# Optimization experiments

Hardware: AMD Instinct MI355X
Metric: run time of the kernel (lower is better)

Reference implementation:

```python
import jax, jax.numpy as jnp
import numpy as np

B, N, D_IN, D_HID, D_OUT = 64, 512, 512, 512, 512


def setup_inputs() -> dict:
    key = jax.random.key(0)
    ks = jax.random.split(key, 8)
    gain = 0.02  # xavier_normal_ gain used in reset_parameters_xavier

    def xavier(k, fan_in, fan_out):
        std = gain * np.sqrt(2.0 / (fan_in + fan_out))
        return jax.random.normal(k, (fan_in, fan_out), dtype=jnp.float32) * std

    return {
        "batch_graph": jax.random.normal(ks[0], (B, N, D_IN), dtype=jnp.float32),
        "adj": jax.random.uniform(ks[1], (B, N, N), dtype=jnp.float32),
        "W1": xavier(ks[2], D_IN, D_HID),
        "b1": jnp.zeros((D_HID,), dtype=jnp.float32),
        "W2": xavier(ks[3], D_HID, D_HID),
        "b2": jnp.zeros((D_HID,), dtype=jnp.float32),
        "W3": xavier(ks[4], D_HID, D_OUT),
        "b3": jnp.zeros((D_OUT,), dtype=jnp.float32),
    }


def _normalize_adj(adj):
    # rowsum^-0.5 with inf -> 0 (original: torch.pow then isinf mask)
    rowsum = adj.sum(axis=1)                       # [B, N] (sum over dim 1, as in torch)
    safe = jnp.where(rowsum == 0, 1.0, rowsum)
    r = jnp.where(rowsum == 0, 0.0, safe ** -0.5)  # [B, N]
    # (adj @ D)^T @ D = D @ adj^T @ D with D = diag(r)
    return r[:, :, None] * jnp.swapaxes(adj, 1, 2) * r[:, None, :]


def reference(batch_graph, adj, W1, b1, W2, b2, W3, b3):
    # Block-diagonal big_adj @ big_graph == per-graph batched matmul.
    A = _normalize_adj(adj)  # [B, N, N]

    def gc(x, W, b):
        # support = x @ W ; output = A @ support + b
        return jnp.einsum('bij,bjd->bid', A, x @ W) + b

    # dropout is identity in eval mode (deterministic reference)
    x = jax.nn.relu(gc(batch_graph, W1, b1))
    x = jax.nn.relu(gc(x, W2, b2))
    return gc(x, W3, b3)  # [B, N, D_OUT]
```

## Files before the change

kernel.cpp:

```cpp
#include <hip/hip_runtime.h>
#include <cstdint>
#include <cstddef>

typedef _Float16 f16;
typedef _Float16 f16x4 __attribute__((ext_vector_type(4)));
typedef _Float16 f16x8 __attribute__((ext_vector_type(8)));
typedef float    f32x4 __attribute__((ext_vector_type(4)));

#define NB 64
#define NN 262144

__device__ __forceinline__ void gload_lds16(const void* g, void* l) {
    __builtin_amdgcn_global_load_lds(
        (const __attribute__((address_space(1))) void*)g,
        (__attribute__((address_space(3))) void*)l, 16, 0, 0);
}

__global__ void k_colsum_part(const float* __restrict__ adj, float* __restrict__ part) {
    int b = blockIdx.y, ch = blockIdx.x;
    const float* ab = adj + (size_t)b * NN + (size_t)ch * 32 * 512;
    int c = threadIdx.x;
    float s0 = 0.f, s1 = 0.f;
    #pragma unroll 8
    for (int i = 0; i < 32; ++i) {
        s0 += ab[i * 512 + c];
        s1 += ab[i * 512 + c + 256];
    }
    float* p = part + ((size_t)b * 16 + ch) * 512;
    p[c] = s0; p[c + 256] = s1;
}

__global__ void k_colsum_fin(const float* __restrict__ part, float* __restrict__ r) {
    int idx = blockIdx.x * 256 + threadIdx.x;
    int b = idx >> 9, n = idx & 511;
    const float* p = part + (size_t)b * 16 * 512 + n;
    float s = 0.f;
    #pragma unroll
    for (int ch = 0; ch < 16; ++ch) s += p[ch * 512];
    r[idx] = (s > 0.f) ? rsqrtf(s) : 0.f;
}

__global__ void k_makeA(const float* __restrict__ adj, const float* __restrict__ r,
                        f16* __restrict__ A_h) {
    __shared__ float t[64][65];
    int b = blockIdx.z;
    int i0 = blockIdx.y * 64, j0 = blockIdx.x * 64;
    const float* ab = adj + (size_t)b * NN;
    int c = threadIdx.x & 63, r4 = threadIdx.x >> 6;
    #pragma unroll
    for (int s = 0; s < 16; ++s) {
        int rr = r4 + s * 4;
        t[rr][c] = ab[(size_t)(j0 + rr) * 512 + i0 + c];
    }
    __syncthreads();
    const float* rb = r + (size_t)b * 512;
    f16* Ab = A_h + (size_t)b * NN;
    int jq = (threadIdx.x & 15) * 4;
    int ib = threadIdx.x >> 4;
    #pragma unroll
    for (int s = 0; s < 4; ++s) {
        int ii = ib + s * 16;
        float ri = 16.f * rb[i0 + ii];
        f16x4 o;
        #pragma unroll
        for (int q = 0; q < 4; ++q)
            o[q] = (f16)(ri * t[jq + q][ii] * rb[j0 + jq + q]);
        *(f16x4*)&Ab[(size_t)(i0 + ii) * 512 + j0 + jq] = o;
    }
}

__global__ void k_transW(const float* __restrict__ W1, const float* __restrict__ W2,
                         const float* __restrict__ W3, f16* __restrict__ Wt) {
    __shared__ float t[64][65];
    const float* W = blockIdx.z == 0 ? W1 : (blockIdx.z == 1 ? W2 : W3);
    f16* out = Wt + (size_t)blockIdx.z * NN;
    int k0 = blockIdx.y * 64, d0 = blockIdx.x * 64;
    int c = threadIdx.x & 63, r4 = threadIdx.x >> 6;
    #pragma unroll
    for (int s = 0; s < 16; ++s) {
        int rr = r4 + s * 4;
        t[rr][c] = W[(size_t)(k0 + rr) * 512 + d0 + c];
    }
    __syncthreads();
    int kq = (threadIdx.x & 15) * 4;
    int db = threadIdx.x >> 4;
    #pragma unroll
    for (int s = 0; s < 4; ++s) {
        int dd = db + s * 16;
        f16x4 o;
        #pragma unroll
        for (int q = 0; q < 4; ++q)
            o[q] = (f16)(64.f * t[kq + q][dd]);
        *(f16x4*)&out[(size_t)(d0 + dd) * 512 + k0 + kq] = o;
    }
}

__global__ void k_cvtX(const float* __restrict__ x, f16* __restrict__ xh) {
    size_t i = ((size_t)blockIdx.x * 256 + threadIdx.x) * 8;
    float4 v0 = *(const float4*)(x + i);
    float4 v1 = *(const float4*)(x + i + 4);
    f16x8 o;
    o[0] = (f16)v0.x; o[1] = (f16)v0.y; o[2] = (f16)v0.z; o[3] = (f16)v0.w;
    o[4] = (f16)v1.x; o[5] = (f16)v1.y; o[6] = (f16)v1.z; o[7] = (f16)v1.w;
    *(f16x8*)(xh + i) = o;
}

template<bool BIAS, bool RELU, bool OUTF32>
__global__ __launch_bounds__(512, 1)
void gemm_tn_ct(const f16* __restrict__ P, size_t pstr,
                const f16* __restrict__ Qt, size_t qstr,
                void* __restrict__ Cout, size_t cstr,
                const float* __restrict__ bias, float iscale, float oscale) {
    __shared__ __align__(16) f16 Plds[2][16384];
    __shared__ __align__(16) f16 Qlds[2][16384];

    const int tid  = threadIdx.x;
    const int lane = tid & 63;
    const int wid  = tid >> 6;
    const int wm   = wid >> 2;
    const int wn   = wid & 3;

    const int wg  = blockIdx.x;
    const int swz = (wg & 7) * 32 + (wg >> 3);
    const int b   = swz >> 2;
    const int tt  = swz & 3;
    const int m0  = (tt >> 1) * 256;
    const int n0  = (tt & 1) * 256;

    const f16* Pb = P + (size_t)b * pstr;
    const f16* Qb = Qt + (size_t)b * qstr;

    const int srow = tid >> 3;
    const int sswz = (tid & 7) ^ (srow & 7);

    const int fr  = lane & 15;
    const int fs  = lane >> 4;
    const int fx  = fr & 7;

    auto stage = [&](const f16* __restrict__ Gb, int row0, f16* lds, int k0) {
        #pragma unroll
        for (int r = 0; r < 4; ++r) {
            const f16* src = Gb + (size_t)(row0 + r * 64 + srow) * 512 + k0 + sswz * 8;
            gload_lds16(src, lds + r * 4096 + tid * 8);
        }
    };

    f32x4 acc[8][4] = {};

    stage(Pb, m0, &Plds[0][0], 0);
    stage(Qb, n0, &Qlds[0][0], 0);

    for (int t = 0; t < 8; ++t) {
        const int nb = t & 1;
        if (t < 7) {
            stage(Pb, m0, &Plds[nb ^ 1][0], (t + 1) * 64);
            stage(Qb, n0, &Qlds[nb ^ 1][0], (t + 1) * 64);
            asm volatile("s_waitcnt vmcnt(8)" ::: "memory");
        } else {
            asm volatile("s_waitcnt vmcnt(0)" ::: "memory");
        }
        __builtin_amdgcn_s_barrier();

        const f16* Pl = &Plds[nb][0];
        const f16* Ql = &Qlds[nb][0];
        #pragma unroll
        for (int krep = 0; krep < 2; ++krep) {
            const int s = fs + krep * 4;
            const int sp = (s ^ fx) * 8;
            f16x8 af[8], bf[4];
            #pragma unroll
            for (int mi = 0; mi < 8; ++mi)
                af[mi] = *(const f16x8*)&Pl[(wm * 128 + mi * 16 + fr) * 64 + sp];
            #pragma unroll
            for (int ni = 0; ni < 4; ++ni)
                bf[ni] = *(const f16x8*)&Ql[(wn * 64 + ni * 16 + fr) * 64 + sp];
            __builtin_amdgcn_s_setprio(1);
            #pragma unroll
            for (int mi = 0; mi < 8; ++mi)
                #pragma unroll
                for (int ni = 0; ni < 4; ++ni)
                    acc[mi][ni] = __builtin_amdgcn_mfma_f32_16x16x32_f16(
                        af[mi], bf[ni], acc[mi][ni], 0, 0, 0);
            __builtin_amdgcn_s_setprio(0);
        }
        asm volatile("s_waitcnt lgkmcnt(0)" ::: "memory");
        __builtin_amdgcn_sched_barrier(0);
        __builtin_amdgcn_s_barrier();
    }

    const int cmb = (lane >> 4) * 4;
    #pragma unroll
    for (int mi = 0; mi < 8; ++mi) {
        #pragma unroll
        for (int ni = 0; ni < 4; ++ni) {
            const int n = n0 + wn * 64 + ni * 16 + fr;
            const int m = m0 + wm * 128 + mi * 16 + cmb;
            float v[4];
            #pragma unroll
            for (int q = 0; q < 4; ++q) {
                float x = acc[mi][ni][q] * iscale;
                if (BIAS) x += bias[m + q];
                if (RELU) x = fmaxf(x, 0.f);
                v[q] = x * oscale;
            }
            if (OUTF32) {
                float* Cb = (float*)Cout + (size_t)b * cstr;
                f32x4 o; o[0] = v[0]; o[1] = v[1]; o[2] = v[2]; o[3] = v[3];
                *(f32x4*)&Cb[(size_t)n * 512 + m] = o;
            } else {
                f16* Cb = (f16*)Cout + (size_t)b * cstr;
                f16x4 o; o[0] = (f16)v[0]; o[1] = (f16)v[1]; o[2] = (f16)v[2]; o[3] = (f16)v[3];
                *(f16x4*)&Cb[(size_t)n * 512 + m] = o;
            }
        }
    }
}

extern "C" void kernel_launch(void* const* d_in, const int* in_sizes, int n_in,
                              void* d_out, int out_size, void* d_ws, size_t ws_size,
                              hipStream_t stream) {
    const float* X0  = (const float*)d_in[0];
    const float* adj = (const float*)d_in[1];
    const float* W1  = (const float*)d_in[2];
    const float* b1  = (const float*)d_in[3];
    const float* W2  = (const float*)d_in[4];
    const float* b2  = (const float*)d_in[5];
    const float* W3  = (const float*)d_in[6];
    const float* b3  = (const float*)d_in[7];

    uint8_t* ws = (uint8_t*)d_ws;
    float* rbuf = (float*)ws;
    f16* Wt1 = (f16*)(ws + 131072);
    f16* Wt2 = Wt1 + NN;
    f16* Wt3 = Wt2 + NN;
    f16* A_h = (f16*)(ws + 131072 + (size_t)3 * NN * 2);
    f16* X_h = A_h + (size_t)NB * NN;
    f16* S_t = X_h + (size_t)NB * NN;
    float* part = (float*)S_t;

    k_colsum_part<<<dim3(16, 64), dim3(256), 0, stream>>>(adj, part);
    k_colsum_fin <<<dim3(128),    dim3(256), 0, stream>>>(part, rbuf);
    k_makeA <<<dim3(8, 8, NB), dim3(256), 0, stream>>>(adj, rbuf, A_h);
    k_transW<<<dim3(8, 8, 3),  dim3(256), 0, stream>>>(W1, W2, W3, Wt1);
    k_cvtX  <<<dim3(8192),     dim3(256), 0, stream>>>(X0, X_h);

    dim3 gg(256), gb(512);
    gemm_tn_ct<false, false, false><<<gg, gb, 0, stream>>>(X_h, (size_t)NN, Wt1, (size_t)0,  S_t, (size_t)NN, nullptr, 1.f, 1.f / 64.f);
    gemm_tn_ct<true,  true,  false><<<gg, gb, 0, stream>>>(S_t, (size_t)NN, A_h, (size_t)NN, X_h, (size_t)NN, b1, 1.f / 16.f, 1.f);
    gemm_tn_ct<false, false, false><<<gg, gb, 0, stream>>>(X_h, (size_t)NN, Wt2, (size_t)0,  S_t, (size_t)NN, nullptr, 1.f, 4.f);
    gemm_tn_ct<true,  true,  false><<<gg, gb, 0, stream>>>(S_t, (size_t)NN, A_h, (size_t)NN, X_h, (size_t)NN, b2, 1.f / 4096.f, 256.f);
    gemm_tn_ct<false, false, false><<<gg, gb, 0, stream>>>(X_h, (size_t)NN, Wt3, (size_t)0,  S_t, (size_t)NN, nullptr, 1.f, 1.f / 64.f);
    gemm_tn_ct<true,  false, true ><<<gg, gb, 0, stream>>>(S_t, (size_t)NN, A_h, (size_t)NN, d_out, (size_t)NN, b3, 1.f / 4096.f, 1.f);
}
```

Before: 222.9 us.

## Shrink GEMM tiles to 128x128 with two blocks per CU and fuse prep kernels

Retiles the batched GEMM from 256x256 tiles with 512 threads and one block per CU to 128x128 tiles with 256 threads and two blocks per CU, launching 1024 blocks. The aim is better occupancy and latency hiding at the cost of lower operand reuse and more LDS/global traffic per flop. It also merges the X conversion, weight transpose and colsum finalize kernels into one launch that dispatches on block index, to cut launch overhead.

```diff
diff --git a/kernel.cpp b/kernel.cpp
--- a/kernel.cpp
+++ b/kernel.cpp
@@ -30,14 +30,53 @@
     p[c] = s0; p[c + 256] = s1;
 }
 
-__global__ void k_colsum_fin(const float* __restrict__ part, float* __restrict__ r) {
-    int idx = blockIdx.x * 256 + threadIdx.x;
-    int b = idx >> 9, n = idx & 511;
-    const float* p = part + (size_t)b * 16 * 512 + n;
-    float s = 0.f;
-    #pragma unroll
-    for (int ch = 0; ch < 16; ++ch) s += p[ch * 512];
-    r[idx] = (s > 0.f) ? rsqrtf(s) : 0.f;
+__global__ void k_prep(const float* __restrict__ X0, f16* __restrict__ X_h,
+                       const float* __restrict__ W1, const float* __restrict__ W2,
+                       const float* __restrict__ W3, f16* __restrict__ Wt,
+                       const float* __restrict__ part, float* __restrict__ r) {
+    const int bid = blockIdx.x;
+    if (bid < 8192) {
+        size_t i = ((size_t)bid * 256 + threadIdx.x) * 8;
+        float4 v0 = *(const float4*)(X0 + i);
+        float4 v1 = *(const float4*)(X0 + i + 4);
+        f16x8 o;
+        o[0] = (f16)v0.x; o[1] = (f16)v0.y; o[2] = (f16)v0.z; o[3] = (f16)v0.w;
+        o[4] = (f16)v1.x; o[5] = (f16)v1.y; o[6] = (f16)v1.z; o[7] = (f16)v1.w;
+        *(f16x8*)(X_h + i) = o;
+    } else if (bid < 8384) {
+        __shared__ float t[64][65];
+        int tt = bid - 8192;
+        int z = tt >> 6, rem = tt & 63;
+        const float* W = z == 0 ? W1 : (z == 1 ? W2 : W3);
+        f16* out = Wt + (size_t)z * NN;
+        int k0 = (rem >> 3) * 64, d0 = (rem & 7) * 64;
+        int c = threadIdx.x & 63, r4 = threadIdx.x >> 6;
+        #pragma unroll
+        for (int s = 0; s < 16; ++s) {
+            int rr = r4 + s * 4;
+            t[rr][c] = W[(size_t)(k0 + rr) * 512 + d0 + c];
+        }
+        __syncthreads();
+        int kq = (threadIdx.x & 15) * 4;
+        int db = threadIdx.x >> 4;
+        #pragma unroll
+        for (int s = 0; s < 4; ++s) {
+            int dd = db + s * 16;
+            f16x4 o;
+            #pragma unroll
+            for (int q = 0; q < 4; ++q)
+                o[q] = (f16)(64.f * t[kq + q][dd]);
+            *(f16x4*)&out[(size_t)(d0 + dd) * 512 + k0 + kq] = o;
+        }
+    } else {
+        int idx = (bid - 8384) * 256 + threadIdx.x;
+        int b = idx >> 9, n = idx & 511;
+        const float* p = part + (size_t)b * 16 * 512 + n;
+        float s = 0.f;
+        #pragma unroll
+        for (int ch = 0; ch < 16; ++ch) s += p[ch * 512];
+        r[idx] = (s > 0.f) ? rsqrtf(s) : 0.f;
+    }
 }
 
 __global__ void k_makeA(const float* __restrict__ adj, const float* __restrict__ r,
@@ -69,63 +108,27 @@
     }
 }
 
-__global__ void k_transW(const float* __restrict__ W1, const float* __restrict__ W2,
-                         const float* __restrict__ W3, f16* __restrict__ Wt) {
-    __shared__ float t[64][65];
-    const float* W = blockIdx.z == 0 ? W1 : (blockIdx.z == 1 ? W2 : W3);
-    f16* out = Wt + (size_t)blockIdx.z * NN;
-    int k0 = blockIdx.y * 64, d0 = blockIdx.x * 64;
-    int c = threadIdx.x & 63, r4 = threadIdx.x >> 6;
-    #pragma unroll
-    for (int s = 0; s < 16; ++s) {
-        int rr = r4 + s * 4;
-        t[rr][c] = W[(size_t)(k0 + rr) * 512 + d0 + c];
-    }
-    __syncthreads();
-    int kq = (threadIdx.x & 15) * 4;
-    int db = threadIdx.x >> 4;
-    #pragma unroll
-    for (int s = 0; s < 4; ++s) {
-        int dd = db + s * 16;
-        f16x4 o;
-        #pragma unroll
-        for (int q = 0; q < 4; ++q)
-            o[q] = (f16)(64.f * t[kq + q][dd]);
-        *(f16x4*)&out[(size_t)(d0 + dd) * 512 + k0 + kq] = o;
-    }
-}
-
-__global__ void k_cvtX(const float* __restrict__ x, f16* __restrict__ xh) {
-    size_t i = ((size_t)blockIdx.x * 256 + threadIdx.x) * 8;
-    float4 v0 = *(const float4*)(x + i);
-    float4 v1 = *(const float4*)(x + i + 4);
-    f16x8 o;
-    o[0] = (f16)v0.x; o[1] = (f16)v0.y; o[2] = (f16)v0.z; o[3] = (f16)v0.w;
-    o[4] = (f16)v1.x; o[5] = (f16)v1.y; o[6] = (f16)v1.z; o[7] = (f16)v1.w;
-    *(f16x8*)(xh + i) = o;
-}
-
 template<bool BIAS, bool RELU, bool OUTF32>
-__global__ __launch_bounds__(512, 1)
+__global__ __launch_bounds__(256, 2)
 void gemm_tn_ct(const f16* __restrict__ P, size_t pstr,
                 const f16* __restrict__ Qt, size_t qstr,
                 void* __restrict__ Cout, size_t cstr,
                 const float* __restrict__ bias, float iscale, float oscale) {
-    __shared__ __align__(16) f16 Plds[2][16384];
-    __shared__ __align__(16) f16 Qlds[2][16384];
+    __shared__ __align__(16) f16 Plds[2][8192];
+    __shared__ __align__(16) f16 Qlds[2][8192];
 
     const int tid  = threadIdx.x;
     const int lane = tid & 63;
     const int wid  = tid >> 6;
-    const int wm   = wid >> 2;
-    const int wn   = wid & 3;
+    const int wm   = wid >> 1;
+    const int wn   = wid & 1;
 
     const int wg  = blockIdx.x;
-    const int swz = (wg & 7) * 32 + (wg >> 3);
-    const int b   = swz >> 2;
-    const int tt  = swz & 3;
-    const int m0  = (tt >> 1) * 256;
-    const int n0  = (tt & 1) * 256;
+    const int swz = (wg & 7) * 128 + (wg >> 3);
+    const int b   = swz >> 4;
+    const int tt  = swz & 15;
+    const int m0  = (tt >> 2) * 128;
+    const int n0  = (tt & 3) * 128;
 
     const f16* Pb = P + (size_t)b * pstr;
     const f16* Qb = Qt + (size_t)b * qstr;
@@ -140,12 +143,12 @@
     auto stage = [&](const f16* __restrict__ Gb, int row0, f16* lds, int k0) {
         #pragma unroll
         for (int r = 0; r < 4; ++r) {
-            const f16* src = Gb + (size_t)(row0 + r * 64 + srow) * 512 + k0 + sswz * 8;
-            gload_lds16(src, lds + r * 4096 + tid * 8);
+            const f16* src = Gb + (size_t)(row0 + r * 32 + srow) * 512 + k0 + sswz * 8;
+            gload_lds16(src, lds + r * 2048 + tid * 8);
         }
     };
 
-    f32x4 acc[8][4] = {};
+    f32x4 acc[4][4] = {};
 
     stage(Pb, m0, &Plds[0][0], 0);
     stage(Qb, n0, &Qlds[0][0], 0);
@@ -165,18 +168,17 @@
         const f16* Ql = &Qlds[nb][0];
         #pragma unroll
         for (int krep = 0; krep < 2; ++krep) {
-            const int s = fs + krep * 4;
-            const int sp = (s ^ fx) * 8;
-            f16x8 af[8], bf[4];
-            #pragma unroll
-            for (int mi = 0; mi < 8; ++mi)
-                af[mi] = *(const f16x8*)&Pl[(wm * 128 + mi * 16 + fr) * 64 + sp];
+            const int sp = ((fs + krep * 4) ^ fx) * 8;
+            f16x8 af[4], bf[4];
+            #pragma unroll
+            for (int mi = 0; mi < 4; ++mi)
+                af[mi] = *(const f16x8*)&Pl[(wm * 64 + mi * 16 + fr) * 64 + sp];
             #pragma unroll
             for (int ni = 0; ni < 4; ++ni)
                 bf[ni] = *(const f16x8*)&Ql[(wn * 64 + ni * 16 + fr) * 64 + sp];
             __builtin_amdgcn_s_setprio(1);
             #pragma unroll
-            for (int mi = 0; mi < 8; ++mi)
+            for (int mi = 0; mi < 4; ++mi)
                 #pragma unroll
                 for (int ni = 0; ni < 4; ++ni)
                     acc[mi][ni] = __builtin_amdgcn_mfma_f32_16x16x32_f16(
@@ -190,11 +192,11 @@
 
     const int cmb = (lane >> 4) * 4;
     #pragma unroll
-    for (int mi = 0; mi < 8; ++mi) {
+    for (int mi = 0; mi < 4; ++mi) {
         #pragma unroll
         for (int ni = 0; ni < 4; ++ni) {
             const int n = n0 + wn * 64 + ni * 16 + fr;
-            const int m = m0 + wm * 128 + mi * 16 + cmb;
+            const int m = m0 + wm * 64 + mi * 16 + cmb;
             float v[4];
             #pragma unroll
             for (int q = 0; q < 4; ++q) {
@@ -239,12 +241,10 @@
     float* part = (float*)S_t;
 
     k_colsum_part<<<dim3(16, 64), dim3(256), 0, stream>>>(adj, part);
-    k_colsum_fin <<<dim3(128),    dim3(256), 0, stream>>>(part, rbuf);
-    k_makeA <<<dim3(8, 8, NB), dim3(256), 0, stream>>>(adj, rbuf, A_h);
-    k_transW<<<dim3(8, 8, 3),  dim3(256), 0, stream>>>(W1, W2, W3, Wt1);
-    k_cvtX  <<<dim3(8192),     dim3(256), 0, stream>>>(X0, X_h);
-
-    dim3 gg(256), gb(512);
+    k_prep <<<dim3(8512),      dim3(256), 0, stream>>>(X0, X_h, W1, W2, W3, Wt1, part, rbuf);
+    k_makeA<<<dim3(8, 8, NB),  dim3(256), 0, stream>>>(adj, rbuf, A_h);
+
+    dim3 gg(1024), gb(256);
     gemm_tn_ct<false, false, false><<<gg, gb, 0, stream>>>(X_h, (size_t)NN, Wt1, (size_t)0,  S_t, (size_t)NN, nullptr, 1.f, 1.f / 64.f);
     gemm_tn_ct<true,  true,  false><<<gg, gb, 0, stream>>>(S_t, (size_t)NN, A_h, (size_t)NN, X_h, (size_t)NN, b1, 1.f / 16.f, 1.f);
     gemm_tn_ct<false, false, false><<<gg, gb, 0, stream>>>(X_h, (size_t)NN, Wt2, (size_t)0,  S_t, (size_t)NN, nullptr, 1.f, 4.f);
```

Result: no change. 227.3 us (+2.0%).

## Fuse X fp32-to-fp16 conversion into first GEMM and merge aux kernels

Applied to the files above, without the earlier changes.

The standalone X conversion kernel is removed. A new 128x128-tile GEMM loads fp32 X directly from global memory, converts it in registers, and writes fp16 into LDS, avoiding an fp16 X round trip through memory. The column-sum-partial and weight-transpose kernels are merged into one launch, which saves a launch. The main GEMM's wait pattern also changes: each stage now waits on vmcnt(0) at the end of the iteration instead of vmcnt(8) before the barrier. That could expose load latency and reduce overlap in the five remaining GEMMs.

```diff
diff --git a/kernel.cpp b/kernel.cpp
--- a/kernel.cpp
+++ b/kernel.cpp
@@ -16,21 +16,51 @@
         (__attribute__((address_space(3))) void*)l, 16, 0, 0);
 }
 
-__global__ void k_colsum_part(const float* __restrict__ adj, float* __restrict__ part) {
-    int b = blockIdx.y, ch = blockIdx.x;
-    const float* ab = adj + (size_t)b * NN + (size_t)ch * 32 * 512;
-    int c = threadIdx.x;
-    float s0 = 0.f, s1 = 0.f;
-    #pragma unroll 8
-    for (int i = 0; i < 32; ++i) {
-        s0 += ab[i * 512 + c];
-        s1 += ab[i * 512 + c + 256];
-    }
-    float* p = part + ((size_t)b * 16 + ch) * 512;
-    p[c] = s0; p[c + 256] = s1;
-}
-
-__global__ void k_colsum_fin(const float* __restrict__ part, float* __restrict__ r) {
+__global__ void k_aux1(const float* __restrict__ adj, float* __restrict__ part,
+                       const float* __restrict__ W1, const float* __restrict__ W2,
+                       const float* __restrict__ W3, f16* __restrict__ Wt) {
+    __shared__ float t[64][65];
+    const int bid = blockIdx.x;
+    if (bid < 1024) {
+        int b = bid >> 4, ch = bid & 15;
+        const float* ab = adj + (size_t)b * NN + (size_t)ch * 32 * 512;
+        int c = threadIdx.x;
+        float s0 = 0.f, s1 = 0.f;
+        #pragma unroll 8
+        for (int i = 0; i < 32; ++i) {
+            s0 += ab[i * 512 + c];
+            s1 += ab[i * 512 + c + 256];
+        }
+        float* p = part + ((size_t)b * 16 + ch) * 512;
+        p[c] = s0; p[c + 256] = s1;
+    } else {
+        int tt = bid - 1024;
+        int z = tt >> 6, rem = tt & 63;
+        const float* W = z == 0 ? W1 : (z == 1 ? W2 : W3);
+        f16* out = Wt + (size_t)z * NN;
+        int k0 = (rem >> 3) * 64, d0 = (rem & 7) * 64;
+        int c = threadIdx.x & 63, r4 = threadIdx.x >> 6;
+        #pragma unroll
+        for (int s = 0; s < 16; ++s) {
+            int rr = r4 + s * 4;
+            t[rr][c] = W[(size_t)(k0 + rr) * 512 + d0 + c];
+        }
+        __syncthreads();
+        int kq = (threadIdx.x & 15) * 4;
+        int db = threadIdx.x >> 4;
+        #pragma unroll
+        for (int s = 0; s < 4; ++s) {
+            int dd = db + s * 16;
+            f16x4 o;
+            #pragma unroll
+            for (int q = 0; q < 4; ++q)
+                o[q] = (f16)(64.f * t[kq + q][dd]);
+            *(f16x4*)&out[(size_t)(d0 + dd) * 512 + k0 + kq] = o;
+        }
+    }
+}
+
+__global__ void k_fin(const float* __restrict__ part, float* __restrict__ r) {
     int idx = blockIdx.x * 256 + threadIdx.x;
     int b = idx >> 9, n = idx & 511;
     const float* p = part + (size_t)b * 16 * 512 + n;
@@ -69,40 +99,122 @@
     }
 }
 
-__global__ void k_transW(const float* __restrict__ W1, const float* __restrict__ W2,
-                         const float* __restrict__ W3, f16* __restrict__ Wt) {
-    __shared__ float t[64][65];
-    const float* W = blockIdx.z == 0 ? W1 : (blockIdx.z == 1 ? W2 : W3);
-    f16* out = Wt + (size_t)blockIdx.z * NN;
-    int k0 = blockIdx.y * 64, d0 = blockIdx.x * 64;
-    int c = threadIdx.x & 63, r4 = threadIdx.x >> 6;
-    #pragma unroll
-    for (int s = 0; s < 16; ++s) {
-        int rr = r4 + s * 4;
-        t[rr][c] = W[(size_t)(k0 + rr) * 512 + d0 + c];
-    }
-    __syncthreads();
-    int kq = (threadIdx.x & 15) * 4;
-    int db = threadIdx.x >> 4;
-    #pragma unroll
-    for (int s = 0; s < 4; ++s) {
-        int dd = db + s * 16;
-        f16x4 o;
-        #pragma unroll
-        for (int q = 0; q < 4; ++q)
-            o[q] = (f16)(64.f * t[kq + q][dd]);
-        *(f16x4*)&out[(size_t)(d0 + dd) * 512 + k0 + kq] = o;
-    }
-}
-
-__global__ void k_cvtX(const float* __restrict__ x, f16* __restrict__ xh) {
-    size_t i = ((size_t)blockIdx.x * 256 + threadIdx.x) * 8;
-    float4 v0 = *(const float4*)(x + i);
-    float4 v1 = *(const float4*)(x + i + 4);
-    f16x8 o;
-    o[0] = (f16)v0.x; o[1] = (f16)v0.y; o[2] = (f16)v0.z; o[3] = (f16)v0.w;
-    o[4] = (f16)v1.x; o[5] = (f16)v1.y; o[6] = (f16)v1.z; o[7] = (f16)v1.w;
-    *(f16x8*)(xh + i) = o;
+__global__ __launch_bounds__(256, 2)
+void gemm_cvt(const float* __restrict__ X0, const f16* __restrict__ Wt,
+              f16* __restrict__ S_t, float oscale) {
+    __shared__ __align__(16) f16 Plds[2][8192];
+    __shared__ __align__(16) f16 Qlds[2][8192];
+
+    const int tid  = threadIdx.x;
+    const int lane = tid & 63;
+    const int wid  = tid >> 6;
+    const int wm   = wid >> 1, wn = wid & 1;
+
+    const int wg  = blockIdx.x;
+    const int swz = (wg & 7) * 128 + (wg >> 3);
+    const int b   = swz >> 4;
+    const int tt  = swz & 15;
+    const int m0  = (tt >> 2) * 128;
+    const int n0  = (tt & 3) * 128;
+
+    const float* Pb = X0 + (size_t)b * NN;
+    const f16*   Qb = Wt;
+
+    const int srow = tid >> 3;
+    const int sswz = (tid & 7) ^ (srow & 7);
+    const int cch  = (tid & 7) ^ ((tid >> 3) & 7);
+
+    const int fr  = lane & 15;
+    const int fs  = lane >> 4;
+    const int fx  = fr & 7;
+
+    auto stageQ = [&](f16* lds, int k0) {
+        #pragma unroll
+        for (int r = 0; r < 4; ++r) {
+            const f16* src = Qb + (size_t)(n0 + r * 32 + srow) * 512 + k0 + sswz * 8;
+            gload_lds16(src, lds + r * 2048 + tid * 8);
+        }
+    };
+    float4 pv[4][2];
+    auto loadP = [&](int k0) {
+        #pragma unroll
+        for (int r = 0; r < 4; ++r) {
+            const float* src = Pb + (size_t)(m0 + r * 32 + (tid >> 3)) * 512 + k0 + cch * 8;
+            pv[r][0] = *(const float4*)src;
+            pv[r][1] = *(const float4*)(src + 4);
+        }
+    };
+    auto writeP = [&](f16* lds) {
+        #pragma unroll
+        for (int r = 0; r < 4; ++r) {
+            f16x8 o;
+            o[0] = (f16)pv[r][0].x; o[1] = (f16)pv[r][0].y;
+            o[2] = (f16)pv[r][0].z; o[3] = (f16)pv[r][0].w;
+            o[4] = (f16)pv[r][1].x; o[5] = (f16)pv[r][1].y;
+            o[6] = (f16)pv[r][1].z; o[7] = (f16)pv[r][1].w;
+            *(f16x8*)(lds + r * 2048 + tid * 8) = o;
+        }
+    };
+
+    f32x4 acc[4][4] = {};
+
+    loadP(0);
+    stageQ(&Qlds[0][0], 0);
+    asm volatile("s_waitcnt vmcnt(4)" ::: "memory");
+    writeP(&Plds[0][0]);
+    asm volatile("s_waitcnt vmcnt(0) lgkmcnt(0)" ::: "memory");
+    __builtin_amdgcn_sched_barrier(0);
+    __builtin_amdgcn_s_barrier();
+
+    for (int t = 0; t < 8; ++t) {
+        const int nb = t & 1;
+        if (t < 7) {
+            loadP((t + 1) * 64);
+            stageQ(&Qlds[nb ^ 1][0], (t + 1) * 64);
+        }
+        const f16* Pl = &Plds[nb][0];
+        const f16* Ql = &Qlds[nb][0];
+        #pragma unroll
+        for (int krep = 0; krep < 2; ++krep) {
+            const int sp = ((fs + krep * 4) ^ fx) * 8;
+            f16x8 af[4], bf[4];
+            #pragma unroll
+            for (int mi = 0; mi < 4; ++mi)
+                af[mi] = *(const f16x8*)&Pl[(wm * 64 + mi * 16 + fr) * 64 + sp];
+            #pragma unroll
+            for (int ni = 0; ni < 4; ++ni)
+                bf[ni] = *(const f16x8*)&Ql[(wn * 64 + ni * 16 + fr) * 64 + sp];
+            __builtin_amdgcn_s_setprio(1);
+            #pragma unroll
+            for (int mi = 0; mi < 4; ++mi)
+                #pragma unroll
+                for (int ni = 0; ni < 4; ++ni)
+                    acc[mi][ni] = __builtin_amdgcn_mfma_f32_16x16x32_f16(
+                        af[mi], bf[ni], acc[mi][ni], 0, 0, 0);
+            __builtin_amdgcn_s_setprio(0);
+        }
+        if (t < 7) {
+            asm volatile("s_waitcnt vmcnt(4)" ::: "memory");
+            writeP(&Plds[nb ^ 1][0]);
+        }
+        asm volatile("s_waitcnt vmcnt(0) lgkmcnt(0)" ::: "memory");
+        __builtin_amdgcn_sched_barrier(0);
+        __builtin_amdgcn_s_barrier();
+    }
+
+    const int cmb = (lane >> 4) * 4;
+    #pragma unroll
+    for (int mi = 0; mi < 4; ++mi) {
+        #pragma unroll
+        for (int ni = 0; ni < 4; ++ni) {
+            const int n = n0 + wn * 64 + ni * 16 + fr;
+            const int m = m0 + wm * 64 + mi * 16 + cmb;
+            f16x4 o;
+            #pragma unroll
+            for (int q = 0; q < 4; ++q) o[q] = (f16)(acc[mi][ni][q] * oscale);
+            *(f16x4*)&S_t[(size_t)b * NN + (size_t)n * 512 + m] = o;
+        }
+    }
 }
 
 template<bool BIAS, bool RELU, bool OUTF32>
@@ -149,24 +261,21 @@
 
     stage(Pb, m0, &Plds[0][0], 0);
     stage(Qb, n0, &Qlds[0][0], 0);
+    asm volatile("s_waitcnt vmcnt(0)" ::: "memory");
+    __builtin_amdgcn_sched_barrier(0);
+    __builtin_amdgcn_s_barrier();
 
     for (int t = 0; t < 8; ++t) {
         const int nb = t & 1;
         if (t < 7) {
             stage(Pb, m0, &Plds[nb ^ 1][0], (t + 1) * 64);
             stage(Qb, n0, &Qlds[nb ^ 1][0], (t + 1) * 64);
-            asm volatile("s_waitcnt vmcnt(8)" ::: "memory");
-        } else {
-            asm volatile("s_waitcnt vmcnt(0)" ::: "memory");
-        }
-        __builtin_amdgcn_s_barrier();
-
+        }
         const f16* Pl = &Plds[nb][0];
         const f16* Ql = &Qlds[nb][0];
         #pragma unroll
         for (int krep = 0; krep < 2; ++krep) {
-            const int s = fs + krep * 4;
-            const int sp = (s ^ fx) * 8;
+            const int sp = ((fs + krep * 4) ^ fx) * 8;
             f16x8 af[8], bf[4];
             #pragma unroll
             for (int mi = 0; mi < 8; ++mi)
@@ -183,7 +292,7 @@
                         af[mi], bf[ni], acc[mi][ni], 0, 0, 0);
             __builtin_amdgcn_s_setprio(0);
         }
-        asm volatile("s_waitcnt lgkmcnt(0)" ::: "memory");
+        asm volatile("s_waitcnt vmcnt(0) lgkmcnt(0)" ::: "memory");
         __builtin_amdgcn_sched_barrier(0);
         __builtin_amdgcn_s_barrier();
     }
@@ -234,21 +343,20 @@
     f16* Wt2 = Wt1 + NN;
     f16* Wt3 = Wt2 + NN;
     f16* A_h = (f16*)(ws + 131072 + (size_t)3 * NN * 2);
-    f16* X_h = A_h + (size_t)NB * NN;
-    f16* S_t = X_h + (size_t)NB * NN;
+    f16* Xa  = A_h + (size_t)NB * NN;
+    f16* S_t = Xa + (size_t)NB * NN;
     float* part = (float*)S_t;
 
-    k_colsum_part<<<dim3(16, 64), dim3(256), 0, stream>>>(adj, part);
-    k_colsum_fin <<<dim3(128),    dim3(256), 0, stream>>>(part, rbuf);
-    k_makeA <<<dim3(8, 8, NB), dim3(256), 0, stream>>>(adj, rbuf, A_h);
-    k_transW<<<dim3(8, 8, 3),  dim3(256), 0, stream>>>(W1, W2, W3, Wt1);
-    k_cvtX  <<<dim3(8192),     dim3(256), 0, stream>>>(X0, X_h);
+    k_aux1 <<<dim3(1216),     dim3(256), 0, stream>>>(adj, part, W1, W2, W3, Wt1);
+    k_fin  <<<dim3(128),      dim3(256), 0, stream>>>(part, rbuf);
+    k_makeA<<<dim3(8, 8, NB), dim3(256), 0, stream>>>(adj, rbuf, A_h);
+
+    gemm_cvt<<<dim3(1024), dim3(256), 0, stream>>>(X0, Wt1, S_t, 1.f / 64.f);
 
     dim3 gg(256), gb(512);
-    gemm_tn_ct<false, false, false><<<gg, gb, 0, stream>>>(X_h, (size_t)NN, Wt1, (size_t)0,  S_t, (size_t)NN, nullptr, 1.f, 1.f / 64.f);
-    gemm_tn_ct<true,  true,  false><<<gg, gb, 0, stream>>>(S_t, (size_t)NN, A_h, (size_t)NN, X_h, (size_t)NN, b1, 1.f / 16.f, 1.f);
-    gemm_tn_ct<false, false, false><<<gg, gb, 0, stream>>>(X_h, (size_t)NN, Wt2, (size_t)0,  S_t, (size_t)NN, nullptr, 1.f, 4.f);
-    gemm_tn_ct<true,  true,  false><<<gg, gb, 0, stream>>>(S_t, (size_t)NN, A_h, (size_t)NN, X_h, (size_t)NN, b2, 1.f / 4096.f, 256.f);
-    gemm_tn_ct<false, false, false><<<gg, gb, 0, stream>>>(X_h, (size_t)NN, Wt3, (size_t)0,  S_t, (size_t)NN, nullptr, 1.f, 1.f / 64.f);
+    gemm_tn_ct<true,  true,  false><<<gg, gb, 0, stream>>>(S_t, (size_t)NN, A_h, (size_t)NN, Xa, (size_t)NN, b1, 1.f / 16.f, 1.f);
+    gemm_tn_ct<false, false, false><<<gg, gb, 0, stream>>>(Xa, (size_t)NN, Wt2, (size_t)0,  S_t, (size_t)NN, nullptr, 1.f, 4.f);
+    gemm_tn_ct<true,  true,  false><<<gg, gb, 0, stream>>>(S_t, (size_t)NN, A_h, (size_t)NN, Xa, (size_t)NN, b2, 1.f / 4096.f, 256.f);
+    gemm_tn_ct<false, false, false><<<gg, gb, 0, stream>>>(Xa, (size_t)NN, Wt3, (size_t)0,  S_t, (size_t)NN, nullptr, 1.f, 1.f / 64.f);
     gemm_tn_ct<true,  false, true ><<<gg, gb, 0, stream>>>(S_t, (size_t)NN, A_h, (size_t)NN, d_out, (size_t)NN, b3, 1.f / 4096.f, 1.f);
 }
```

Measured after the change: 223.6 us. About the same (+0.3%).
